# Kernel optimization log

Measured on AMD Instinct MI355X. Metric: run time of the kernel, lower is better.

The kernel has to match this reference:

```python
import jax, jax.numpy as jnp
import numpy as np

VOCAB, D = 50000, 256
B, R, C, T = 4, 64, 64, 32


def setup_inputs() -> dict:
    key = jax.random.key(0)
    k1, k2, k3 = jax.random.split(key, 3)
    x = jax.random.randint(k1, (B, R, C, T), 0, VOCAB, dtype=jnp.int32)
    E = jax.random.normal(k2, (VOCAB, D), dtype=jnp.float32)
    W = jax.random.normal(k3, (D,), dtype=jnp.float32) * (1.0 / np.sqrt(D))
    b = jnp.zeros((1,), dtype=jnp.float32)
    return {"x": x, "E": E, "W": W, "b": b}


def reference(x, E, W, b):
    # Fused version of the per-cell Python loop:
    #   embed tokens, sum over token dim, (dropout = identity in eval), linear -> scalar per cell.
    emb_sum = E[x].sum(axis=3)                      # [B, R, C, D]
    scores = jnp.einsum("brcd,d->brc", emb_sum, W) + b[0]  # [B, R, C]
    return scores
```

## Files before the change

### kernel.cpp

```cpp
#include <hip/hip_runtime.h>

#define VOCAB_SZ 50000
#define EMB_D    256
#define N_CELLS  (4 * 64 * 64)
#define TOK_T    32

__global__ void __launch_bounds__(256)
vocab_dot_kernel(const float* __restrict__ E, const float* __restrict__ W,
                 float* __restrict__ s) {
    const int tid    = blockIdx.x * blockDim.x + threadIdx.x;
    const int wave   = tid >> 6;
    const int lane   = threadIdx.x & 63;
    const int sub    = lane & 15;
    const int grp    = lane >> 4;
    const int nwaves = (gridDim.x * blockDim.x) >> 6;

    const float4 w0 = *reinterpret_cast<const float4*>(W +   0 + sub * 4);
    const float4 w1 = *reinterpret_cast<const float4*>(W +  64 + sub * 4);
    const float4 w2 = *reinterpret_cast<const float4*>(W + 128 + sub * 4);
    const float4 w3 = *reinterpret_cast<const float4*>(W + 192 + sub * 4);

    const int ngroups = VOCAB_SZ / 4;
    for (int g = wave; g < ngroups; g += nwaves) {
        const int row = g * 4 + grp;
        const float* er = E + (size_t)row * EMB_D;
        const float4 e0 = *reinterpret_cast<const float4*>(er +   0 + sub * 4);
        const float4 e1 = *reinterpret_cast<const float4*>(er +  64 + sub * 4);
        const float4 e2 = *reinterpret_cast<const float4*>(er + 128 + sub * 4);
        const float4 e3 = *reinterpret_cast<const float4*>(er + 192 + sub * 4);

        float p = e0.x*w0.x + e0.y*w0.y + e0.z*w0.z + e0.w*w0.w;
        p      += e1.x*w1.x + e1.y*w1.y + e1.z*w1.z + e1.w*w1.w;
        p      += e2.x*w2.x + e2.y*w2.y + e2.z*w2.z + e2.w*w2.w;
        p      += e3.x*w3.x + e3.y*w3.y + e3.z*w3.z + e3.w*w3.w;

        p += __shfl_xor(p, 1);
        p += __shfl_xor(p, 2);
        p += __shfl_xor(p, 4);
        p += __shfl_xor(p, 8);

        if (sub == 0) s[row] = p;
    }
}

__global__ void __launch_bounds__(256)
cell_sum_kernel(const int* __restrict__ x, const float* __restrict__ s,
                const float* __restrict__ b, float* __restrict__ out) {
    const int tid = blockIdx.x * blockDim.x + threadIdx.x;
    if (tid >= N_CELLS * (TOK_T / 4)) return;

    const int4 v = reinterpret_cast<const int4*>(x)[tid];
    float acc = s[v.x] + s[v.y] + s[v.z] + s[v.w];

    acc += __shfl_xor(acc, 1);
    acc += __shfl_xor(acc, 2);
    acc += __shfl_xor(acc, 4);

    if ((threadIdx.x & 7) == 0) out[tid >> 3] = acc + b[0];
}

extern "C" void kernel_launch(void* const* d_in, const int* in_sizes, int n_in,
                              void* d_out, int out_size, void* d_ws, size_t ws_size,
                              hipStream_t stream) {
    const int*   x = (const int*)d_in[0];
    const float* E = (const float*)d_in[1];
    const float* W = (const float*)d_in[2];
    const float* b = (const float*)d_in[3];
    float* out = (float*)d_out;
    float* s   = (float*)d_ws;

    vocab_dot_kernel<<<1024, 256, 0, stream>>>(E, W, s);

    cell_sum_kernel<<<512, 256, 0, stream>>>(x, s, b, out);
}
```

Before: 93.09 us.

## Fuse vocab dot and cell sum into one cooperative kernel with grid sync

Merges the two kernels into a single cooperative launch. A grid-wide sync separates the per-vocab dot-product phase from the per-cell gather-sum phase. Each thread now handles two tokens instead of four so that 1024x256 threads cover all tokens. This removes one kernel launch and its inter-kernel gap, but adds the cost of a grid barrier and of a cooperative launch, which needs all 1024 blocks to be resident at once.

New measurement: 186.0 us. 99.8% more time.

```diff
diff --git a/kernel.cpp b/kernel.cpp
--- a/kernel.cpp
+++ b/kernel.cpp
@@ -1,19 +1,26 @@
 #include <hip/hip_runtime.h>
+#include <hip/hip_cooperative_groups.h>
 
-#define VOCAB_SZ 50000
-#define EMB_D    256
-#define N_CELLS  (4 * 64 * 64)
-#define TOK_T    32
+namespace cg = cooperative_groups;
 
-__global__ void __launch_bounds__(256)
-vocab_dot_kernel(const float* __restrict__ E, const float* __restrict__ W,
-                 float* __restrict__ s) {
-    const int tid    = blockIdx.x * blockDim.x + threadIdx.x;
-    const int wave   = tid >> 6;
-    const int lane   = threadIdx.x & 63;
-    const int sub    = lane & 15;
-    const int grp    = lane >> 4;
-    const int nwaves = (gridDim.x * blockDim.x) >> 6;
+#define VOCAB_SZ      50000
+#define EMB_D         256
+#define N_CELLS       16384
+#define TOK_T         32
+#define N_TOKENS      (N_CELLS * TOK_T)
+#define GRID_BLOCKS   1024
+#define BLOCK_THREADS 256
+
+__global__ void __launch_bounds__(BLOCK_THREADS, 4)
+fused_kernel(const int* __restrict__ x, const float* __restrict__ E,
+             const float* __restrict__ W, const float* __restrict__ b,
+             float* __restrict__ out, float* __restrict__ s) {
+    const int tid  = blockIdx.x * blockDim.x + threadIdx.x;
+    const int lane = threadIdx.x & 63;
+    const int sub  = lane & 15;
+    const int grp  = lane >> 4;
+    const int wave = tid >> 6;
+    const int nwaves = (GRID_BLOCKS * BLOCK_THREADS) >> 6;
 
     const float4 w0 = *reinterpret_cast<const float4*>(W +   0 + sub * 4);
     const float4 w1 = *reinterpret_cast<const float4*>(W +  64 + sub * 4);
@@ -41,22 +48,18 @@
 
         if (sub == 0) s[row] = p;
     }
-}
 
-__global__ void __launch_bounds__(256)
-cell_sum_kernel(const int* __restrict__ x, const float* __restrict__ s,
-                const float* __restrict__ b, float* __restrict__ out) {
-    const int tid = blockIdx.x * blockDim.x + threadIdx.x;
-    if (tid >= N_CELLS * (TOK_T / 4)) return;
+    cg::this_grid().sync();
 
-    const int4 v = reinterpret_cast<const int4*>(x)[tid];
-    float acc = s[v.x] + s[v.y] + s[v.z] + s[v.w];
+    const int2 v = reinterpret_cast<const int2*>(x)[tid];
+    float acc = s[v.x] + s[v.y];
 
     acc += __shfl_xor(acc, 1);
     acc += __shfl_xor(acc, 2);
     acc += __shfl_xor(acc, 4);
+    acc += __shfl_xor(acc, 8);
 
-    if ((threadIdx.x & 7) == 0) out[tid >> 3] = acc + b[0];
+    if (sub == 0) out[tid >> 4] = acc + b[0];
 }
 
 extern "C" void kernel_launch(void* const* d_in, const int* in_sizes, int n_in,
@@ -69,7 +72,9 @@
     float* out = (float*)d_out;
     float* s   = (float*)d_ws;
 
-    vocab_dot_kernel<<<1024, 256, 0, stream>>>(E, W, s);
-
-    cell_sum_kernel<<<512, 256, 0, stream>>>(x, s, b, out);
+    void* args[] = { (void*)&x, (void*)&E, (void*)&W, (void*)&b,
+                     (void*)&out, (void*)&s };
+    hipLaunchCooperativeKernel((const void*)fused_kernel,
+                               dim3(GRID_BLOCKS), dim3(BLOCK_THREADS),
+                               args, 0, stream);
 }
```
